# Performance work log

Measured on AMD Instinct MI355X. Metric: run time of the kernel, lower is better.

## Reference

```python
import jax, jax.numpy as jnp
import numpy as np


def _position_table(seq_len, d_model, dtype):
    # position[i, j] = sin(i / 10000**((j+1)/d))  if j even
    #                  cos(i / 10000**((j+1)/d))  if j odd
    # (note the nonstandard (j+1)/d exponent, faithful to the source)
    i = jnp.arange(seq_len, dtype=dtype)[:, None]          # [S, 1]
    j = jnp.arange(d_model, dtype=dtype)[None, :]          # [1, D]
    pf = i / jnp.power(jnp.asarray(10000.0, dtype), (j + 1.0) / d_model)  # [S, D]
    even = (jnp.arange(d_model) % 2 == 0)[None, :]
    return jnp.where(even, jnp.sin(pf), jnp.cos(pf))       # [S, D]


def setup_inputs() -> dict:
    key = jax.random.key(0)
    x = jax.random.normal(key, (4, 8192, 1024), dtype=jnp.float32)
    return {"x": x}


def reference(x) -> jnp.ndarray:
    B, S, D = x.shape
    pos = _position_table(S, D, x.dtype)
    return x + pos[None, :, :]
```

## Files before the change

kernel.cpp:

```cpp
#include <hip/hip_runtime.h>
#include <math.h>

#define PE_S 8192
#define PE_D 1024
#define PE_B 4

__global__ __launch_bounds__(256) void position_encoder_kernel(
    const float* __restrict__ x, float* __restrict__ out) {
    const int tid = blockIdx.x * blockDim.x + threadIdx.x;
    const int d4  = tid & (PE_D / 4 - 1);
    const int s   = tid >> 8;
    const int d0  = d4 << 2;

    const float fs = (float)s;
    const float a2 = -0.012976281620653760f;
    const float w0 = exp2f((float)(d0 + 1) * a2);
    const float w1 = exp2f((float)(d0 + 2) * a2);
    const float w2 = exp2f((float)(d0 + 3) * a2);
    const float w3 = exp2f((float)(d0 + 4) * a2);

    float4 p;
    p.x = sinf(fs * w0);
    p.y = cosf(fs * w1);
    p.z = sinf(fs * w2);
    p.w = cosf(fs * w3);

    const size_t base  = (size_t)s * PE_D + (size_t)d0;
    const size_t plane = (size_t)PE_S * PE_D;
#pragma unroll
    for (int b = 0; b < PE_B; ++b) {
        const float4 v = *reinterpret_cast<const float4*>(x + (size_t)b * plane + base);
        float4 o;
        o.x = v.x + p.x;
        o.y = v.y + p.y;
        o.z = v.z + p.z;
        o.w = v.w + p.w;
        *reinterpret_cast<float4*>(out + (size_t)b * plane + base) = o;
    }
}

extern "C" void kernel_launch(void* const* d_in, const int* in_sizes, int n_in,
                              void* d_out, int out_size, void* d_ws, size_t ws_size,
                              hipStream_t stream) {
    const float* x = (const float*)d_in[0];
    float* out = (float*)d_out;

    const int threads = 256;
    const int total_quads = PE_S * PE_D / 4;
    const int blocks = total_quads / threads;
    position_encoder_kernel<<<blocks, threads, 0, stream>>>(x, out);
}
```

Before: 231.5 us.

## Use hardware sin/cos with turn-based range reduction, 8 elements per thread, nontemporal stores

Each thread now handles 8 consecutive features instead of 4, so half as many threads are launched and each issues two 16-byte loads and stores per batch. The sinf/cosf library calls are replaced by the hardware v_sin/v_cos builtins. The phase is converted to turns by folding a 1/(2π) factor into the exp2 exponent, then reduced to its fractional part with floorf. Output stores become nontemporal to avoid polluting cache. The cost is accuracy: large arguments lose precision after fp32 range reduction in turns, and the per-thread access pattern changes from one float4 to two adjacent float4s.

```diff
diff --git a/kernel.cpp b/kernel.cpp
--- a/kernel.cpp
+++ b/kernel.cpp
@@ -5,37 +5,43 @@
 #define PE_D 1024
 #define PE_B 4
 
+typedef float v4f __attribute__((ext_vector_type(4)));
+
 __global__ __launch_bounds__(256) void position_encoder_kernel(
     const float* __restrict__ x, float* __restrict__ out) {
     const int tid = blockIdx.x * blockDim.x + threadIdx.x;
-    const int d4  = tid & (PE_D / 4 - 1);
-    const int s   = tid >> 8;
-    const int d0  = d4 << 2;
+    const int oct = tid & (PE_D / 8 - 1);
+    const int s   = tid >> 7;
+    const int d0  = oct << 3;
 
     const float fs = (float)s;
     const float a2 = -0.012976281620653760f;
-    const float w0 = exp2f((float)(d0 + 1) * a2);
-    const float w1 = exp2f((float)(d0 + 2) * a2);
-    const float w2 = exp2f((float)(d0 + 3) * a2);
-    const float w3 = exp2f((float)(d0 + 4) * a2);
+    const float c2 = -2.6514961294723187f;
 
-    float4 p;
-    p.x = sinf(fs * w0);
-    p.y = cosf(fs * w1);
-    p.z = sinf(fs * w2);
-    p.w = cosf(fs * w3);
+    float p[8];
+#pragma unroll
+    for (int k = 0; k < 8; k += 2) {
+        const float we = __builtin_amdgcn_exp2f((float)(d0 + k + 1) * a2 + c2);
+        const float wo = __builtin_amdgcn_exp2f((float)(d0 + k + 2) * a2 + c2);
+        float te = fs * we;  te -= floorf(te);
+        float to = fs * wo;  to -= floorf(to);
+        p[k]     = __builtin_amdgcn_sinf(te);
+        p[k + 1] = __builtin_amdgcn_cosf(to);
+    }
+
+    const v4f pe0 = {p[0], p[1], p[2], p[3]};
+    const v4f pe1 = {p[4], p[5], p[6], p[7]};
 
     const size_t base  = (size_t)s * PE_D + (size_t)d0;
     const size_t plane = (size_t)PE_S * PE_D;
 #pragma unroll
     for (int b = 0; b < PE_B; ++b) {
-        const float4 v = *reinterpret_cast<const float4*>(x + (size_t)b * plane + base);
-        float4 o;
-        o.x = v.x + p.x;
-        o.y = v.y + p.y;
-        o.z = v.z + p.z;
-        o.w = v.w + p.w;
-        *reinterpret_cast<float4*>(out + (size_t)b * plane + base) = o;
+        const v4f* xp = reinterpret_cast<const v4f*>(x + (size_t)b * plane + base);
+        v4f* op       = reinterpret_cast<v4f*>(out + (size_t)b * plane + base);
+        const v4f v0 = xp[0];
+        const v4f v1 = xp[1];
+        __builtin_nontemporal_store(v0 + pe0, op);
+        __builtin_nontemporal_store(v1 + pe1, op + 1);
     }
 }
 
@@ -46,7 +52,7 @@
     float* out = (float*)d_out;
 
     const int threads = 256;
-    const int total_quads = PE_S * PE_D / 4;
-    const int blocks = total_quads / threads;
+    const int total = PE_S * (PE_D / 8);
+    const int blocks = total / threads;
     position_encoder_kernel<<<blocks, threads, 0, stream>>>(x, out);
 }
```

After: 267.0 us. +15.3%, slower.
